# Kernel tuning notes

Hardware: AMD Instinct MI355X
Metric: run time of the kernel (lower is better)

The kernel has to match this reference:

```python
import jax, jax.numpy as jnp
import numpy as np

N = 100000          # nodes
E = 3200000         # edges
C_IN = 64
HIDDEN = 64
NUM_CLASSES = 10
NUM_GRAPHS = 256
EPS = 1e-5


def _graph_conv(x, src, dst, w_rel, w_root, b):
    # PyG GraphConv(aggr='mean'): out_i = W_rel * mean_{j->i} x_j + W_root * x_i + b
    msg_sum = jax.ops.segment_sum(x[src], dst, num_segments=N)            # [N, C]
    cnt = jax.ops.segment_sum(jnp.ones((src.shape[0], 1), x.dtype), dst,
                              num_segments=N)                             # [N, 1]
    agg = msg_sum / jnp.maximum(cnt, 1.0)
    return agg @ w_rel + x @ w_root + b


def _batch_norm(x, gamma, beta):
    # PyG BatchNorm in training mode: batch stats over the node dimension
    mean = jnp.mean(x, axis=0)
    var = jnp.var(x, axis=0)
    return (x - mean) * jax.lax.rsqrt(var + EPS) * gamma + beta


def setup_inputs() -> dict:
    key = jax.random.key(0)
    ks = jax.random.split(key, 20)
    x = jax.random.normal(ks[0], (N, C_IN), dtype=jnp.float32)
    edge_index = jax.random.randint(ks[1], (2, E), 0, N, dtype=jnp.int32)
    batch = jnp.sort(jax.random.randint(ks[2], (N,), 0, NUM_GRAPHS, dtype=jnp.int32))

    def lin(k, fan_in, fan_out):
        s = 1.0 / np.sqrt(fan_in)
        return jax.random.uniform(k, (fan_in, fan_out), jnp.float32, -s, s)

    dims = [(C_IN, 16), (16, 32), (32, 32), (32, HIDDEN)]
    params = {}
    ki = 3
    for i, (ci, co) in enumerate(dims, start=1):
        params[f"w_rel{i}"] = lin(ks[ki], ci, co); ki += 1
        params[f"w_root{i}"] = lin(ks[ki], ci, co); ki += 1
        params[f"b{i}"] = jnp.zeros((co,), jnp.float32)
        params[f"g{i}"] = jnp.ones((co,), jnp.float32)
        params[f"be{i}"] = jnp.zeros((co,), jnp.float32)
    params["w_lin1"] = lin(ks[ki], HIDDEN, HIDDEN); ki += 1
    params["b_lin1"] = jnp.zeros((HIDDEN,), jnp.float32)
    params["w_lin2"] = lin(ks[ki], HIDDEN, NUM_CLASSES); ki += 1
    params["b_lin2"] = jnp.zeros((NUM_CLASSES,), jnp.float32)

    return {"x": x, "edge_index": edge_index, "batch": batch, **params}


def reference(x, edge_index, batch,
              w_rel1, w_root1, b1, g1, be1,
              w_rel2, w_root2, b2, g2, be2,
              w_rel3, w_root3, b3, g3, be3,
              w_rel4, w_root4, b4, g4, be4,
              w_lin1, b_lin1, w_lin2, b_lin2):
    src, dst = edge_index[0], edge_index[1]
    h = jax.nn.elu(_batch_norm(_graph_conv(x, src, dst, w_rel1, w_root1, b1), g1, be1))
    h = jax.nn.elu(_batch_norm(_graph_conv(h, src, dst, w_rel2, w_root2, b2), g2, be2))
    h = jax.nn.elu(_batch_norm(_graph_conv(h, src, dst, w_rel3, w_root3, b3), g3, be3))
    h = jax.nn.elu(_batch_norm(_graph_conv(h, src, dst, w_rel4, w_root4, b4), g4, be4))
    # global mean pool over graphs
    pooled = jax.ops.segment_sum(h, batch, num_segments=NUM_GRAPHS)
    cnt = jax.ops.segment_sum(jnp.ones((N, 1), h.dtype), batch, num_segments=NUM_GRAPHS)
    pooled = pooled / jnp.maximum(cnt, 1.0)
    z = jax.nn.relu(pooled @ w_lin1 + b_lin1)
    # dropout omitted (deterministic / eval mode)
    logits = z @ w_lin2 + b_lin2
    return jax.nn.log_softmax(logits, axis=-1)
```

## Files before the change

kernel.cpp:

```cpp
#include <hip/hip_runtime.h>
#include <hip/hip_bf16.h>
#include <math.h>

#define NGRAPHS 256
#define BSHIFT 8
#define NBUCK 512
#define NSORT 256
#define SBLK 256
#define SMASK 0x00FFFFFFu

__device__ __forceinline__ float bf2f(unsigned short u) {
    return __uint_as_float((unsigned)u << 16);
}
__device__ __forceinline__ unsigned short f2bf(float f) {
    unsigned u = __float_as_uint(f);
    unsigned r = (u + 0x7FFFu + ((u >> 16) & 1u)) >> 16;
    return (unsigned short)r;
}

__global__ __launch_bounds__(256) void k_bhist(const int* __restrict__ dst, int* __restrict__ hmat, int E) {
    __shared__ int hist[NBUCK];
    for (int i = threadIdx.x; i < NBUCK; i += 256) hist[i] = 0;
    __syncthreads();
    int chunk = (E + NSORT - 1) / NSORT;
    int lo = blockIdx.x * chunk;
    int hi = lo + chunk; if (hi > E) hi = E;
    for (int i = lo + threadIdx.x; i < hi; i += 256) {
        int d = __builtin_nontemporal_load(dst + i);
        atomicAdd(&hist[d >> BSHIFT], 1);
    }
    __syncthreads();
    for (int i = threadIdx.x; i < NBUCK; i += 256)
        hmat[(size_t)blockIdx.x * NBUCK + i] = hist[i];
}

__global__ __launch_bounds__(256) void k_cscan(int* __restrict__ hmat, int* __restrict__ btot) {
    int col = blockIdx.x * 256 + threadIdx.x;
    int run = 0;
#pragma unroll 4
    for (int r = 0; r < NSORT; r++) {
        int v = hmat[(size_t)r * NBUCK + col];
        hmat[(size_t)r * NBUCK + col] = run;
        run += v;
    }
    btot[col] = run;
}

__global__ __launch_bounds__(512) void k_bscan(const int* __restrict__ btot, int* __restrict__ bstart) {
    __shared__ int s[512];
    int tid = threadIdx.x;
    int v = btot[tid];
    s[tid] = v;
    __syncthreads();
    for (int off = 1; off < 512; off <<= 1) {
        int t = (tid >= off) ? s[tid - off] : 0;
        __syncthreads();
        s[tid] += t;
        __syncthreads();
    }
    bstart[tid] = s[tid] - v;
    if (tid == 511) bstart[NBUCK] = s[511];
}

__global__ __launch_bounds__(256) void k_bscatter(const int* __restrict__ src, const int* __restrict__ dst,
                                                  const int* __restrict__ hmat, const int* __restrict__ bstart,
                                                  unsigned* __restrict__ ebuf, int E) {
    __shared__ int cur[NBUCK];
    for (int i = threadIdx.x; i < NBUCK; i += 256)
        cur[i] = bstart[i] + hmat[(size_t)blockIdx.x * NBUCK + i];
    __syncthreads();
    int chunk = (E + NSORT - 1) / NSORT;
    int lo = blockIdx.x * chunk;
    int hi = lo + chunk; if (hi > E) hi = E;
    for (int i = lo + threadIdx.x; i < hi; i += 256) {
        int d = __builtin_nontemporal_load(dst + i);
        int s = __builtin_nontemporal_load(src + i);
        int p = atomicAdd(&cur[d >> BSHIFT], 1);
        ebuf[p] = (unsigned)s | ((unsigned)(d & 255) << 24);
    }
}

__global__ __launch_bounds__(256) void k_sort2(const unsigned* __restrict__ ebuf, const int* __restrict__ bstart,
                                               int* __restrict__ csr, int* __restrict__ row_start, int N) {
    __shared__ int hist[256];
    __shared__ int sc[256];
    __shared__ int scur[256];
    int b = blockIdx.x;
    int e0 = bstart[b], e1 = bstart[b + 1];
    hist[threadIdx.x] = 0;
    __syncthreads();
    for (int i = e0 + threadIdx.x; i < e1; i += 256)
        atomicAdd(&hist[__builtin_nontemporal_load(ebuf + i) >> 24], 1);
    __syncthreads();
    sc[threadIdx.x] = hist[threadIdx.x];
    __syncthreads();
    for (int off = 1; off < 256; off <<= 1) {
        int t = (threadIdx.x >= off) ? sc[threadIdx.x - off] : 0;
        __syncthreads();
        sc[threadIdx.x] += t;
        __syncthreads();
    }
    {
        int inc = sc[threadIdx.x];
        int ex = inc - hist[threadIdx.x];
        scur[threadIdx.x] = e0 + ex;
        int node = (b << BSHIFT) + threadIdx.x;
        if (node < N) row_start[node] = e0 + ex;
        if (node == N - 1) row_start[N] = e0 + inc;
    }
    __syncthreads();
    for (int i = e0 + threadIdx.x; i < e1; i += 256) {
        unsigned w = __builtin_nontemporal_load(ebuf + i);
        int p = atomicAdd(&scur[w >> 24], 1);
        csr[p] = (int)(w & SMASK);
    }
}

template <int CI, int CO, bool HAS_REL, bool HAS_ROOT, bool ADD_AGG, bool HAS_BIAS, bool IN_BF16, bool OUT_BF16>
__global__ __launch_bounds__(256) void k_lin(const void* __restrict__ hroot_v, const float* __restrict__ hrel,
                                             const float* __restrict__ w_rel, const float* __restrict__ w_root,
                                             const float* __restrict__ bias, const float* __restrict__ aggadd,
                                             float* __restrict__ out, unsigned short* __restrict__ outb, int N) {
    constexpr int QPR = CO / 4;
    __shared__ float s_rel[HAS_REL ? CI * CO : 1];
    __shared__ float s_root[HAS_ROOT ? CI * CO : 1];
    __shared__ float s_b[HAS_BIAS ? CO : 4];
    if (HAS_REL)
        for (int i = threadIdx.x; i < CI * CO; i += 256) s_rel[i] = w_rel[i];
    if (HAS_ROOT)
        for (int i = threadIdx.x; i < CI * CO; i += 256) s_root[i] = w_root[i];
    if (HAS_BIAS && threadIdx.x < CO) s_b[threadIdx.x] = bias[threadIdx.x];
    __syncthreads();

    int t = blockIdx.x * 256 + threadIdx.x;
    int n = t / QPR;
    int c0 = (t % QPR) * 4;
    if (n >= N) return;

    float rr[HAS_ROOT ? CI : 1];
    if (HAS_ROOT) {
        if (IN_BF16) {
            const ushort4* hp = (const ushort4*)((const unsigned short*)hroot_v + (size_t)n * CI);
#pragma unroll
            for (int i = 0; i < CI / 4; i++) {
                ushort4 v = hp[i];
                rr[4 * i + 0] = bf2f(v.x); rr[4 * i + 1] = bf2f(v.y);
                rr[4 * i + 2] = bf2f(v.z); rr[4 * i + 3] = bf2f(v.w);
            }
        } else {
            const float4* hp = (const float4*)((const float*)hroot_v + (size_t)n * CI);
#pragma unroll
            for (int i = 0; i < CI / 4; i++) {
                float4 v = hp[i];
                rr[4 * i + 0] = v.x; rr[4 * i + 1] = v.y; rr[4 * i + 2] = v.z; rr[4 * i + 3] = v.w;
            }
        }
    }
    float ar[HAS_REL ? CI : 1];
    if (HAS_REL) {
        const float4* mp = (const float4*)(hrel + (size_t)n * CI);
#pragma unroll
        for (int i = 0; i < CI / 4; i++) {
            float4 v = mp[i];
            ar[4 * i + 0] = v.x; ar[4 * i + 1] = v.y; ar[4 * i + 2] = v.z; ar[4 * i + 3] = v.w;
        }
    }

    float4 acc;
    if (HAS_BIAS) acc = *(const float4*)&s_b[c0];
    else { acc.x = 0.f; acc.y = 0.f; acc.z = 0.f; acc.w = 0.f; }
    if (ADD_AGG) {
        float4 v = *(const float4*)(aggadd + (size_t)n * CO + c0);
        acc.x += v.x; acc.y += v.y; acc.z += v.z; acc.w += v.w;
    }

#pragma unroll
    for (int ci = 0; ci < CI; ci++) {
        if (HAS_REL) {
            float a = ar[ci];
            float4 w = *(const float4*)&s_rel[ci * CO + c0];
            acc.x += a * w.x; acc.y += a * w.y; acc.z += a * w.z; acc.w += a * w.w;
        }
        if (HAS_ROOT) {
            float hv = rr[ci];
            float4 w = *(const float4*)&s_root[ci * CO + c0];
            acc.x += hv * w.x; acc.y += hv * w.y; acc.z += hv * w.z; acc.w += hv * w.w;
        }
    }
    if (OUT_BF16) {
        ushort4 o;
        o.x = f2bf(acc.x); o.y = f2bf(acc.y); o.z = f2bf(acc.z); o.w = f2bf(acc.w);
        *(ushort4*)(outb + (size_t)n * CO + c0) = o;
    } else {
        *(float4*)(out + (size_t)n * CO + c0) = acc;
    }
}

#define GCHUNK 1024
template <int C>
__global__ __launch_bounds__(256) void k_gather(const unsigned short* __restrict__ h,
                                                const int* __restrict__ row_start,
                                                const int* __restrict__ csr, float* __restrict__ agg, int N) {
    constexpr int LPR = C / 4;
    constexpr int EPP = 64 / LPR;
    constexpr int DEPTH = 32 / EPP;
    __shared__ int sbuf[GCHUNK];
    int lane = threadIdx.x & 63;
    int w = threadIdx.x >> 6;
    int nb = blockIdx.x * 4;
    int wid = nb + w;
    bool act = wid < N;
    int nb_end = nb + 4; if (nb_end > N) nb_end = N;
    int eb0 = row_start[nb];
    int eb1 = row_start[nb_end];
    int r0 = act ? row_start[wid] : 0;
    int r1 = act ? row_start[wid + 1] : 0;
    int es = lane / LPR;
    int cq = (lane % LPR) * 4;

    float a0 = 0.f, a1 = 0.f, a2 = 0.f, a3 = 0.f;
    for (int base = eb0; base < eb1; base += GCHUNK) {
        int len = eb1 - base; if (len > GCHUNK) len = GCHUNK;
        __syncthreads();
        for (int i = threadIdx.x; i < len; i += 256)
            sbuf[i] = __builtin_nontemporal_load(csr + base + i);
        __syncthreads();
        if (act) {
            int lo = (r0 > base ? r0 : base) - base;
            int hiv = r1 < base + len ? r1 : base + len;
            int hi = hiv - base;
            if (hi > lo) {
                int nfull = (hi - lo) >> 5;
                int j0 = lo;
                for (int b = 0; b < nfull; b++, j0 += 32) {
                    int s[DEPTH];
#pragma unroll
                    for (int u = 0; u < DEPTH; u++) s[u] = sbuf[j0 + u * EPP + es];
                    ushort4 v[DEPTH];
#pragma unroll
                    for (int u = 0; u < DEPTH; u++)
                        v[u] = *(const ushort4*)(h + (size_t)s[u] * C + cq);
#pragma unroll
                    for (int u = 0; u < DEPTH; u++) {
                        a0 += bf2f(v[u].x); a1 += bf2f(v[u].y);
                        a2 += bf2f(v[u].z); a3 += bf2f(v[u].w);
                    }
                }
                for (int j = j0 + es; j < hi; j += EPP) {
                    int s = sbuf[j];
                    ushort4 v = *(const ushort4*)(h + (size_t)s * C + cq);
                    a0 += bf2f(v.x); a1 += bf2f(v.y); a2 += bf2f(v.z); a3 += bf2f(v.w);
                }
            }
        }
    }
#pragma unroll
    for (int off = LPR; off < 64; off <<= 1) {
        a0 += __shfl_xor(a0, off, 64);
        a1 += __shfl_xor(a1, off, 64);
        a2 += __shfl_xor(a2, off, 64);
        a3 += __shfl_xor(a3, off, 64);
    }
    if (act && lane < LPR) {
        int deg = r1 - r0;
        float rec = 1.0f / (float)(deg > 0 ? deg : 1);
        float4 o; o.x = a0 * rec; o.y = a1 * rec; o.z = a2 * rec; o.w = a3 * rec;
        *(float4*)(agg + (size_t)wid * C + cq) = o;
    }
}

template <int CO>
__global__ __launch_bounds__(256) void k_stats(const float* __restrict__ h, float* __restrict__ partials,
                                               const float* __restrict__ g, const float* __restrict__ be,
                                               float* __restrict__ stats, int* __restrict__ cnt,
                                               float invN, int N) {
    constexpr int QPR = CO / 4;
    __shared__ float part[4][2 * CO];
    __shared__ float red[128];
    __shared__ int is_last;
    int total = N * QPR;
    float s0 = 0, s1 = 0, s2 = 0, s3 = 0, q0 = 0, q1 = 0, q2 = 0, q3 = 0;
    int idx = blockIdx.x * 256 + threadIdx.x;
    for (int i = idx; i < total; i += SBLK * 256) {
        float4 v = ((const float4*)h)[i];
        s0 += v.x; q0 += v.x * v.x;
        s1 += v.y; q1 += v.y * v.y;
        s2 += v.z; q2 += v.z * v.z;
        s3 += v.w; q3 += v.w * v.w;
    }
#pragma unroll
    for (int off = QPR; off < 64; off <<= 1) {
        s0 += __shfl_xor(s0, off, 64); q0 += __shfl_xor(q0, off, 64);
        s1 += __shfl_xor(s1, off, 64); q1 += __shfl_xor(q1, off, 64);
        s2 += __shfl_xor(s2, off, 64); q2 += __shfl_xor(q2, off, 64);
        s3 += __shfl_xor(s3, off, 64); q3 += __shfl_xor(q3, off, 64);
    }
    int lane = threadIdx.x & 63;
    int w = threadIdx.x >> 6;
    if (lane < QPR) {
        int cq = lane * 4;
        part[w][cq + 0] = s0; part[w][CO + cq + 0] = q0;
        part[w][cq + 1] = s1; part[w][CO + cq + 1] = q1;
        part[w][cq + 2] = s2; part[w][CO + cq + 2] = q2;
        part[w][cq + 3] = s3; part[w][CO + cq + 3] = q3;
    }
    __syncthreads();
    if (threadIdx.x < 2 * CO) {
        float v = part[0][threadIdx.x] + part[1][threadIdx.x] + part[2][threadIdx.x] + part[3][threadIdx.x];
        partials[blockIdx.x * (2 * CO) + threadIdx.x] = v;
    }
    __threadfence();
    if (threadIdx.x == 0) is_last = (atomicAdd(cnt, 1) == SBLK - 1);
    __syncthreads();
    if (!is_last) return;
    __threadfence();
    int c = threadIdx.x;
    if (c < 2 * CO) {
        float s = 0.f;
        for (int b = 0; b < SBLK; b++) s += partials[b * 2 * CO + c];
        red[c] = s;
    }
    __syncthreads();
    if (c < CO) {
        float mean = red[c] * invN;
        float var = red[CO + c] * invN - mean * mean;
        float sc = g[c] * rsqrtf(var + 1e-5f);
        stats[128 + c] = sc;
        stats[192 + c] = be[c] - mean * sc;
    }
}

template <int CO>
__global__ __launch_bounds__(256) void k_bn_elu(const float* __restrict__ h, const float* __restrict__ stats,
                                                unsigned short* __restrict__ hb, int N) {
    __shared__ float sc[CO], sh[CO];
    if (threadIdx.x < CO) {
        sc[threadIdx.x] = stats[128 + threadIdx.x];
        sh[threadIdx.x] = stats[192 + threadIdx.x];
    }
    __syncthreads();
    int total = N * (CO / 4);
    int i = blockIdx.x * 256 + threadIdx.x;
    if (i >= total) return;
    float4 v = ((const float4*)h)[i];
    int cq = (i % (CO / 4)) * 4;
    v.x = v.x * sc[cq + 0] + sh[cq + 0];
    v.y = v.y * sc[cq + 1] + sh[cq + 1];
    v.z = v.z * sc[cq + 2] + sh[cq + 2];
    v.w = v.w * sc[cq + 3] + sh[cq + 3];
    v.x = v.x > 0.f ? v.x : expm1f(v.x);
    v.y = v.y > 0.f ? v.y : expm1f(v.y);
    v.z = v.z > 0.f ? v.z : expm1f(v.z);
    v.w = v.w > 0.f ? v.w : expm1f(v.w);
    ushort4 o;
    o.x = f2bf(v.x); o.y = f2bf(v.y); o.z = f2bf(v.z); o.w = f2bf(v.w);
    ((ushort4*)hb)[i] = o;
}

__global__ __launch_bounds__(256) void k_bn_elu_pool(const float* __restrict__ h, const float* __restrict__ stats,
                                                     const int* __restrict__ batch,
                                                     float* __restrict__ pooled, float* __restrict__ cntg, int N) {
    int lane = threadIdx.x & 63;
    int wid = blockIdx.x * 4 + (threadIdx.x >> 6);
    int n0 = wid * 16;
    if (n0 >= N) return;
    float scl = stats[128 + lane];
    float shl = stats[192 + lane];
    int nmax = N - n0; if (nmax > 16) nmax = 16;
    int cur = batch[n0];
    float acc = 0.f;
    float run = 0.f;
    for (int k = 0; k < nmax; k++) {
        int g = batch[n0 + k];
        if (g != cur) {
            atomicAdd(&pooled[(size_t)cur * 64 + lane], acc);
            if (lane == 0) atomicAdd(&cntg[cur], run);
            cur = g; acc = 0.f; run = 0.f;
        }
        float v = h[(size_t)(n0 + k) * 64 + lane] * scl + shl;
        v = v > 0.f ? v : expm1f(v);
        acc += v;
        run += 1.f;
    }
    atomicAdd(&pooled[(size_t)cur * 64 + lane], acc);
    if (lane == 0) atomicAdd(&cntg[cur], run);
}

__global__ __launch_bounds__(256) void k_head(const float* __restrict__ pooled, const float* __restrict__ cntg,
                                              const float* __restrict__ w1, const float* __restrict__ b1,
                                              const float* __restrict__ w2, const float* __restrict__ b2,
                                              float* __restrict__ out) {
    int g = threadIdx.x;
    float rec = 1.0f / fmaxf(cntg[g], 1.0f);
    float p[64];
    {
        const float4* pp = (const float4*)(pooled + (size_t)g * 64);
#pragma unroll
        for (int i = 0; i < 16; i++) {
            float4 v = pp[i];
            p[4 * i + 0] = v.x * rec; p[4 * i + 1] = v.y * rec;
            p[4 * i + 2] = v.z * rec; p[4 * i + 3] = v.w * rec;
        }
    }
    float lg[10];
#pragma unroll
    for (int t = 0; t < 10; t++) lg[t] = b2[t];
#pragma unroll 1
    for (int j = 0; j < 64; j++) {
        float a = b1[j];
#pragma unroll
        for (int k = 0; k < 64; k++) a += p[k] * w1[k * 64 + j];
        a = fmaxf(a, 0.f);
#pragma unroll
        for (int t = 0; t < 10; t++) lg[t] += a * w2[j * 10 + t];
    }
    float m = -1e30f;
#pragma unroll
    for (int t = 0; t < 10; t++) m = fmaxf(m, lg[t]);
    float s = 0.f;
#pragma unroll
    for (int t = 0; t < 10; t++) s += expf(lg[t] - m);
    float lse = m + logf(s);
#pragma unroll
    for (int t = 0; t < 10; t++) out[(size_t)g * 10 + t] = lg[t] - lse;
}

extern "C" void kernel_launch(void* const* d_in, const int* in_sizes, int n_in,
                              void* d_out, int out_size, void* d_ws, size_t ws_size,
                              hipStream_t stream) {
    const float* x = (const float*)d_in[0];
    const int* ei = (const int*)d_in[1];
    const int* batch = (const int*)d_in[2];
    const int N = in_sizes[0] / 64;
    const int E = in_sizes[1] / 2;
    const int* src = ei;
    const int* dst = ei + E;

    const float* w_rel1 = (const float*)d_in[3];
    const float* w_root1 = (const float*)d_in[4];
    const float* b1 = (const float*)d_in[5];
    const float* g1 = (const float*)d_in[6];
    const float* be1 = (const float*)d_in[7];
    const float* w_rel2 = (const float*)d_in[8];
    const float* w_root2 = (const float*)d_in[9];
    const float* b2 = (const float*)d_in[10];
    const float* g2 = (const float*)d_in[11];
    const float* be2 = (const float*)d_in[12];
    const float* w_rel3 = (const float*)d_in[13];
    const float* w_root3 = (const float*)d_in[14];
    const float* b3 = (const float*)d_in[15];
    const float* g3 = (const float*)d_in[16];
    const float* be3 = (const float*)d_in[17];
    const float* w_rel4 = (const float*)d_in[18];
    const float* w_root4 = (const float*)d_in[19];
    const float* b4 = (const float*)d_in[20];
    const float* g4 = (const float*)d_in[21];
    const float* be4 = (const float*)d_in[22];
    const float* w_lin1 = (const float*)d_in[23];
    const float* b_lin1 = (const float*)d_in[24];
    const float* w_lin2 = (const float*)d_in[25];
    const float* b_lin2 = (const float*)d_in[26];

    char* ws = (char*)d_ws;
    size_t off = 0;
    auto alloc = [&](size_t bytes) { size_t o = off; off += (bytes + 255) & ~(size_t)255; return o; };
    int* hmat = (int*)(ws + alloc((size_t)NSORT * NBUCK * 4));
    int* btot = (int*)(ws + alloc((size_t)NBUCK * 4));
    int* bstart = (int*)(ws + alloc((size_t)(NBUCK + 1) * 4));
    unsigned* ebuf = (unsigned*)(ws + alloc((size_t)E * 4));
    int* csr = (int*)(ws + alloc((size_t)E * 4));
    int* row_start = (int*)(ws + alloc((size_t)(N + 1) * 4));
    float* agg = (float*)(ws + alloc((size_t)N * 32 * 4));
    unsigned short* y1b = (unsigned short*)(ws + alloc((size_t)N * 16 * 2));
    unsigned short* hb = (unsigned short*)(ws + alloc((size_t)N * 64 * 2));
    float* bufA = (float*)(ws + alloc((size_t)N * 64 * 4));
    float* stats = (float*)(ws + alloc(4 * 256 * 4));
    float* partials = (float*)(ws + alloc((size_t)SBLK * 128 * 4));
    float* pooled = (float*)(ws + alloc((size_t)(NGRAPHS * 64 + NGRAPHS + 8) * 4));
    float* cntg = pooled + NGRAPHS * 64;
    int* cnt = (int*)(cntg + NGRAPHS);

    hipMemsetAsync(pooled, 0, (size_t)(NGRAPHS * 64 + NGRAPHS + 8) * 4, stream);

    const float invN = 1.0f / (float)N;
    const int gbl = (N + 3) / 4;
    auto lgrid = [&](int qpr) { return (N * qpr + 255) / 256; };

    k_bhist<<<NSORT, 256, 0, stream>>>(dst, hmat, E);
    k_cscan<<<NBUCK / 256, 256, 0, stream>>>(hmat, btot);
    k_bscan<<<1, 512, 0, stream>>>(btot, bstart);
    k_bscatter<<<NSORT, 256, 0, stream>>>(src, dst, hmat, bstart, ebuf, E);
    k_sort2<<<NBUCK, 256, 0, stream>>>(ebuf, bstart, csr, row_start, N);

    k_lin<64, 16, true, false, false, false, false, true><<<lgrid(4), 256, 0, stream>>>(
        nullptr, x, w_rel1, nullptr, nullptr, nullptr, nullptr, y1b, N);
    k_gather<16><<<gbl, 256, 0, stream>>>(y1b, row_start, csr, agg, N);
    k_lin<64, 16, false, true, true, true, false, false><<<lgrid(4), 256, 0, stream>>>(
        x, nullptr, nullptr, w_root1, b1, agg, bufA, nullptr, N);
    k_stats<16><<<SBLK, 256, 0, stream>>>(bufA, partials, g1, be1, stats + 0, cnt + 0, invN, N);
    k_bn_elu<16><<<(N * 4 + 255) / 256, 256, 0, stream>>>(bufA, stats + 0, hb, N);

    k_gather<16><<<gbl, 256, 0, stream>>>(hb, row_start, csr, agg, N);
    k_lin<16, 32, true, true, false, true, true, false><<<lgrid(8), 256, 0, stream>>>(
        hb, agg, w_rel2, w_root2, b2, nullptr, bufA, nullptr, N);
    k_stats<32><<<SBLK, 256, 0, stream>>>(bufA, partials, g2, be2, stats + 256, cnt + 1, invN, N);
    k_bn_elu<32><<<(N * 8 + 255) / 256, 256, 0, stream>>>(bufA, stats + 256, hb, N);

    k_gather<32><<<gbl, 256, 0, stream>>>(hb, row_start, csr, agg, N);
    k_lin<32, 32, true, true, false, true, true, false><<<lgrid(8), 256, 0, stream>>>(
        hb, agg, w_rel3, w_root3, b3, nullptr, bufA, nullptr, N);
    k_stats<32><<<SBLK, 256, 0, stream>>>(bufA, partials, g3, be3, stats + 512, cnt + 2, invN, N);
    k_bn_elu<32><<<(N * 8 + 255) / 256, 256, 0, stream>>>(bufA, stats + 512, hb, N);

    k_gather<32><<<gbl, 256, 0, stream>>>(hb, row_start, csr, agg, N);
    k_lin<32, 64, true, true, false, true, true, false><<<lgrid(16), 256, 0, stream>>>(
        hb, agg, w_rel4, w_root4, b4, nullptr, bufA, nullptr, N);
    k_stats<64><<<SBLK, 256, 0, stream>>>(bufA, partials, g4, be4, stats + 768, cnt + 3, invN, N);
    int waves16 = (N + 15) / 16;
    k_bn_elu_pool<<<(waves16 + 3) / 4, 256, 0, stream>>>(bufA, stats + 768, batch, pooled, cntg, N);

    k_head<<<1, 256, 0, stream>>>(pooled, cntg, w_lin1, b_lin1, w_lin2, b_lin2, (float*)d_out);
}
```

Before: 638.9 us.

## Fuse BN stats into linear kernels, merge scans, head into pool, drop memset

Computes BatchNorm sum and sum-of-squares inside the linear kernel, which now runs as a grid-stride loop over 512 blocks, so the separate stats pass that re-read the layer output is gone. The column and bucket scans become one kernel, the memset is moved into the histogram kernel's first block, and the head MLP runs in the last block of the pooling kernel. The gather loop is also rewritten with predicated batches of four. This cuts launches and one full read of each layer output, at the cost of a persistent-grid linear kernel with less parallelism and a serial last-block reduction.

```diff
diff --git a/kernel.cpp b/kernel.cpp
--- a/kernel.cpp
+++ b/kernel.cpp
@@ -6,7 +6,7 @@
 #define BSHIFT 8
 #define NBUCK 512
 #define NSORT 256
-#define SBLK 256
+#define LSTAT 512
 #define SMASK 0x00FFFFFFu
 
 __device__ __forceinline__ float bf2f(unsigned short u) {
@@ -18,7 +18,11 @@
     return (unsigned short)r;
 }
 
-__global__ __launch_bounds__(256) void k_bhist(const int* __restrict__ dst, int* __restrict__ hmat, int E) {
+__global__ __launch_bounds__(256) void k_bhist(const int* __restrict__ dst, int* __restrict__ hmat, int E,
+                                               float* __restrict__ zbase, int zwords) {
+    if (blockIdx.x == 0) {
+        for (int i = threadIdx.x; i < zwords; i += 256) zbase[i] = 0.f;
+    }
     __shared__ int hist[NBUCK];
     for (int i = threadIdx.x; i < NBUCK; i += 256) hist[i] = 0;
     __syncthreads();
@@ -34,8 +38,9 @@
         hmat[(size_t)blockIdx.x * NBUCK + i] = hist[i];
 }
 
-__global__ __launch_bounds__(256) void k_cscan(int* __restrict__ hmat, int* __restrict__ btot) {
-    int col = blockIdx.x * 256 + threadIdx.x;
+__global__ __launch_bounds__(512) void k_scan(int* __restrict__ hmat, int* __restrict__ bstart) {
+    __shared__ int s[512];
+    int col = threadIdx.x;
     int run = 0;
 #pragma unroll 4
     for (int r = 0; r < NSORT; r++) {
@@ -43,23 +48,16 @@
         hmat[(size_t)r * NBUCK + col] = run;
         run += v;
     }
-    btot[col] = run;
-}
-
-__global__ __launch_bounds__(512) void k_bscan(const int* __restrict__ btot, int* __restrict__ bstart) {
-    __shared__ int s[512];
-    int tid = threadIdx.x;
-    int v = btot[tid];
-    s[tid] = v;
+    s[col] = run;
     __syncthreads();
     for (int off = 1; off < 512; off <<= 1) {
-        int t = (tid >= off) ? s[tid - off] : 0;
+        int t = (col >= off) ? s[col - off] : 0;
         __syncthreads();
-        s[tid] += t;
+        s[col] += t;
         __syncthreads();
     }
-    bstart[tid] = s[tid] - v;
-    if (tid == 511) bstart[NBUCK] = s[511];
+    bstart[col] = s[col] - run;
+    if (col == 511) bstart[NBUCK] = s[511];
 }
 
 __global__ __launch_bounds__(256) void k_bscatter(const int* __restrict__ src, const int* __restrict__ dst,
@@ -116,83 +114,151 @@
     }
 }
 
-template <int CI, int CO, bool HAS_REL, bool HAS_ROOT, bool ADD_AGG, bool HAS_BIAS, bool IN_BF16, bool OUT_BF16>
-__global__ __launch_bounds__(256) void k_lin(const void* __restrict__ hroot_v, const float* __restrict__ hrel,
-                                             const float* __restrict__ w_rel, const float* __restrict__ w_root,
-                                             const float* __restrict__ bias, const float* __restrict__ aggadd,
-                                             float* __restrict__ out, unsigned short* __restrict__ outb, int N) {
+template <int CI, int CO>
+__global__ __launch_bounds__(256) void k_lin_rel(const float* __restrict__ hrel, const float* __restrict__ w_rel,
+                                                 unsigned short* __restrict__ outb, int N) {
     constexpr int QPR = CO / 4;
-    __shared__ float s_rel[HAS_REL ? CI * CO : 1];
-    __shared__ float s_root[HAS_ROOT ? CI * CO : 1];
-    __shared__ float s_b[HAS_BIAS ? CO : 4];
-    if (HAS_REL)
-        for (int i = threadIdx.x; i < CI * CO; i += 256) s_rel[i] = w_rel[i];
-    if (HAS_ROOT)
-        for (int i = threadIdx.x; i < CI * CO; i += 256) s_root[i] = w_root[i];
-    if (HAS_BIAS && threadIdx.x < CO) s_b[threadIdx.x] = bias[threadIdx.x];
-    __syncthreads();
-
+    __shared__ float s_rel[CI * CO];
+    for (int i = threadIdx.x; i < CI * CO; i += 256) s_rel[i] = w_rel[i];
+    __syncthreads();
     int t = blockIdx.x * 256 + threadIdx.x;
     int n = t / QPR;
     int c0 = (t % QPR) * 4;
     if (n >= N) return;
-
-    float rr[HAS_ROOT ? CI : 1];
-    if (HAS_ROOT) {
+    float ar[CI];
+    const float4* mp = (const float4*)(hrel + (size_t)n * CI);
+#pragma unroll
+    for (int i = 0; i < CI / 4; i++) {
+        float4 v = mp[i];
+        ar[4 * i + 0] = v.x; ar[4 * i + 1] = v.y; ar[4 * i + 2] = v.z; ar[4 * i + 3] = v.w;
+    }
+    float4 acc; acc.x = 0.f; acc.y = 0.f; acc.z = 0.f; acc.w = 0.f;
+#pragma unroll
+    for (int ci = 0; ci < CI; ci++) {
+        float a = ar[ci];
+        float4 w = *(const float4*)&s_rel[ci * CO + c0];
+        acc.x += a * w.x; acc.y += a * w.y; acc.z += a * w.z; acc.w += a * w.w;
+    }
+    ushort4 o;
+    o.x = f2bf(acc.x); o.y = f2bf(acc.y); o.z = f2bf(acc.z); o.w = f2bf(acc.w);
+    *(ushort4*)(outb + (size_t)n * CO + c0) = o;
+}
+
+template <int CI, int CO, bool HAS_REL, bool ADD_AGG, bool IN_BF16>
+__global__ __launch_bounds__(256) void k_lin_stats(const void* __restrict__ hroot_v, const float* __restrict__ hrel,
+                                                   const float* __restrict__ w_rel, const float* __restrict__ w_root,
+                                                   const float* __restrict__ bias, const float* __restrict__ aggadd,
+                                                   float* __restrict__ out, float* __restrict__ partials,
+                                                   const float* __restrict__ g, const float* __restrict__ be,
+                                                   float* __restrict__ stats, int* __restrict__ cnt,
+                                                   float invN, int N) {
+    constexpr int QPR = CO / 4;
+    __shared__ float s_rel[HAS_REL ? CI * CO : 1];
+    __shared__ float s_root[CI * CO];
+    __shared__ float s_b[CO];
+    __shared__ float part[4][2 * CO];
+    __shared__ float red[128];
+    __shared__ int is_last;
+    if (HAS_REL)
+        for (int i = threadIdx.x; i < CI * CO; i += 256) s_rel[i] = w_rel[i];
+    for (int i = threadIdx.x; i < CI * CO; i += 256) s_root[i] = w_root[i];
+    if (threadIdx.x < CO) s_b[threadIdx.x] = bias[threadIdx.x];
+    __syncthreads();
+
+    int total = N * QPR;
+    float s0 = 0, s1 = 0, s2 = 0, s3 = 0, q0 = 0, q1 = 0, q2 = 0, q3 = 0;
+    for (int i = blockIdx.x * 256 + threadIdx.x; i < total; i += LSTAT * 256) {
+        int n = i / QPR;
+        int c0 = (i % QPR) * 4;
+
+        float rr[CI];
         if (IN_BF16) {
             const ushort4* hp = (const ushort4*)((const unsigned short*)hroot_v + (size_t)n * CI);
 #pragma unroll
-            for (int i = 0; i < CI / 4; i++) {
-                ushort4 v = hp[i];
-                rr[4 * i + 0] = bf2f(v.x); rr[4 * i + 1] = bf2f(v.y);
-                rr[4 * i + 2] = bf2f(v.z); rr[4 * i + 3] = bf2f(v.w);
+            for (int k = 0; k < CI / 4; k++) {
+                ushort4 v = hp[k];
+                rr[4 * k + 0] = bf2f(v.x); rr[4 * k + 1] = bf2f(v.y);
+                rr[4 * k + 2] = bf2f(v.z); rr[4 * k + 3] = bf2f(v.w);
             }
         } else {
             const float4* hp = (const float4*)((const float*)hroot_v + (size_t)n * CI);
 #pragma unroll
-            for (int i = 0; i < CI / 4; i++) {
-                float4 v = hp[i];
-                rr[4 * i + 0] = v.x; rr[4 * i + 1] = v.y; rr[4 * i + 2] = v.z; rr[4 * i + 3] = v.w;
+            for (int k = 0; k < CI / 4; k++) {
+                float4 v = hp[k];
+                rr[4 * k + 0] = v.x; rr[4 * k + 1] = v.y; rr[4 * k + 2] = v.z; rr[4 * k + 3] = v.w;
             }
         }
-    }
-    float ar[HAS_REL ? CI : 1];
-    if (HAS_REL) {
-        const float4* mp = (const float4*)(hrel + (size_t)n * CI);
-#pragma unroll
-        for (int i = 0; i < CI / 4; i++) {
-            float4 v = mp[i];
-            ar[4 * i + 0] = v.x; ar[4 * i + 1] = v.y; ar[4 * i + 2] = v.z; ar[4 * i + 3] = v.w;
-        }
-    }
-
-    float4 acc;
-    if (HAS_BIAS) acc = *(const float4*)&s_b[c0];
-    else { acc.x = 0.f; acc.y = 0.f; acc.z = 0.f; acc.w = 0.f; }
-    if (ADD_AGG) {
-        float4 v = *(const float4*)(aggadd + (size_t)n * CO + c0);
-        acc.x += v.x; acc.y += v.y; acc.z += v.z; acc.w += v.w;
-    }
-
-#pragma unroll
-    for (int ci = 0; ci < CI; ci++) {
+        float ar[HAS_REL ? CI : 1];
         if (HAS_REL) {
-            float a = ar[ci];
-            float4 w = *(const float4*)&s_rel[ci * CO + c0];
-            acc.x += a * w.x; acc.y += a * w.y; acc.z += a * w.z; acc.w += a * w.w;
-        }
-        if (HAS_ROOT) {
+            const float4* mp = (const float4*)(hrel + (size_t)n * CI);
+#pragma unroll
+            for (int k = 0; k < CI / 4; k++) {
+                float4 v = mp[k];
+                ar[4 * k + 0] = v.x; ar[4 * k + 1] = v.y; ar[4 * k + 2] = v.z; ar[4 * k + 3] = v.w;
+            }
+        }
+        float4 acc = *(const float4*)&s_b[c0];
+        if (ADD_AGG) {
+            float4 v = ((const float4*)aggadd)[i];
+            acc.x += v.x; acc.y += v.y; acc.z += v.z; acc.w += v.w;
+        }
+#pragma unroll
+        for (int ci = 0; ci < CI; ci++) {
             float hv = rr[ci];
             float4 w = *(const float4*)&s_root[ci * CO + c0];
             acc.x += hv * w.x; acc.y += hv * w.y; acc.z += hv * w.z; acc.w += hv * w.w;
-        }
-    }
-    if (OUT_BF16) {
-        ushort4 o;
-        o.x = f2bf(acc.x); o.y = f2bf(acc.y); o.z = f2bf(acc.z); o.w = f2bf(acc.w);
-        *(ushort4*)(outb + (size_t)n * CO + c0) = o;
-    } else {
-        *(float4*)(out + (size_t)n * CO + c0) = acc;
+            if (HAS_REL) {
+                float a = ar[ci];
+                float4 wr = *(const float4*)&s_rel[ci * CO + c0];
+                acc.x += a * wr.x; acc.y += a * wr.y; acc.z += a * wr.z; acc.w += a * wr.w;
+            }
+        }
+        ((float4*)out)[i] = acc;
+        s0 += acc.x; q0 += acc.x * acc.x;
+        s1 += acc.y; q1 += acc.y * acc.y;
+        s2 += acc.z; q2 += acc.z * acc.z;
+        s3 += acc.w; q3 += acc.w * acc.w;
+    }
+#pragma unroll
+    for (int off = QPR; off < 64; off <<= 1) {
+        s0 += __shfl_xor(s0, off, 64); q0 += __shfl_xor(q0, off, 64);
+        s1 += __shfl_xor(s1, off, 64); q1 += __shfl_xor(q1, off, 64);
+        s2 += __shfl_xor(s2, off, 64); q2 += __shfl_xor(q2, off, 64);
+        s3 += __shfl_xor(s3, off, 64); q3 += __shfl_xor(q3, off, 64);
+    }
+    int lane = threadIdx.x & 63;
+    int w = threadIdx.x >> 6;
+    if (lane < QPR) {
+        int cq = lane * 4;
+        part[w][cq + 0] = s0; part[w][CO + cq + 0] = q0;
+        part[w][cq + 1] = s1; part[w][CO + cq + 1] = q1;
+        part[w][cq + 2] = s2; part[w][CO + cq + 2] = q2;
+        part[w][cq + 3] = s3; part[w][CO + cq + 3] = q3;
+    }
+    __syncthreads();
+    if (threadIdx.x < 2 * CO) {
+        float v = part[0][threadIdx.x] + part[1][threadIdx.x] + part[2][threadIdx.x] + part[3][threadIdx.x];
+        partials[blockIdx.x * (2 * CO) + threadIdx.x] = v;
+    }
+    __threadfence();
+    if (threadIdx.x == 0) is_last = (atomicAdd(cnt, 1) == LSTAT - 1);
+    __syncthreads();
+    if (!is_last) return;
+    __threadfence();
+    int c = threadIdx.x;
+    if (c < 2 * CO) {
+        float s = 0.f;
+#pragma unroll 8
+        for (int b = 0; b < LSTAT; b++) s += partials[b * 2 * CO + c];
+        red[c] = s;
+    }
+    __syncthreads();
+    if (c < CO) {
+        float mean = red[c] * invN;
+        float var = red[CO + c] * invN - mean * mean;
+        float sc = g[c] * rsqrtf(var + 1e-5f);
+        stats[128 + c] = sc;
+        stats[192 + c] = be[c] - mean * sc;
     }
 }
 
@@ -203,7 +269,7 @@
                                                 const int* __restrict__ csr, float* __restrict__ agg, int N) {
     constexpr int LPR = C / 4;
     constexpr int EPP = 64 / LPR;
-    constexpr int DEPTH = 32 / EPP;
+    constexpr int BATCH = 4 * EPP;
     __shared__ int sbuf[GCHUNK];
     int lane = threadIdx.x & 63;
     int w = threadIdx.x >> 6;
@@ -229,27 +295,25 @@
             int lo = (r0 > base ? r0 : base) - base;
             int hiv = r1 < base + len ? r1 : base + len;
             int hi = hiv - base;
-            if (hi > lo) {
-                int nfull = (hi - lo) >> 5;
-                int j0 = lo;
-                for (int b = 0; b < nfull; b++, j0 += 32) {
-                    int s[DEPTH];
-#pragma unroll
-                    for (int u = 0; u < DEPTH; u++) s[u] = sbuf[j0 + u * EPP + es];
-                    ushort4 v[DEPTH];
-#pragma unroll
-                    for (int u = 0; u < DEPTH; u++)
-                        v[u] = *(const ushort4*)(h + (size_t)s[u] * C + cq);
-#pragma unroll
-                    for (int u = 0; u < DEPTH; u++) {
+#pragma unroll 2
+            for (int j0 = lo; j0 < hi; j0 += BATCH) {
+                int s[4]; bool p[4];
+#pragma unroll
+                for (int u = 0; u < 4; u++) {
+                    int j = j0 + u * EPP + es;
+                    p[u] = j < hi;
+                    s[u] = sbuf[p[u] ? j : j0];
+                }
+                ushort4 v[4];
+#pragma unroll
+                for (int u = 0; u < 4; u++)
+                    v[u] = *(const ushort4*)(h + (size_t)s[u] * C + cq);
+#pragma unroll
+                for (int u = 0; u < 4; u++) {
+                    if (p[u]) {
                         a0 += bf2f(v[u].x); a1 += bf2f(v[u].y);
                         a2 += bf2f(v[u].z); a3 += bf2f(v[u].w);
                     }
-                }
-                for (int j = j0 + es; j < hi; j += EPP) {
-                    int s = sbuf[j];
-                    ushort4 v = *(const ushort4*)(h + (size_t)s * C + cq);
-                    a0 += bf2f(v.x); a1 += bf2f(v.y); a2 += bf2f(v.z); a3 += bf2f(v.w);
                 }
             }
         }
@@ -266,67 +330,6 @@
         float rec = 1.0f / (float)(deg > 0 ? deg : 1);
         float4 o; o.x = a0 * rec; o.y = a1 * rec; o.z = a2 * rec; o.w = a3 * rec;
         *(float4*)(agg + (size_t)wid * C + cq) = o;
-    }
-}
-
-template <int CO>
-__global__ __launch_bounds__(256) void k_stats(const float* __restrict__ h, float* __restrict__ partials,
-                                               const float* __restrict__ g, const float* __restrict__ be,
-                                               float* __restrict__ stats, int* __restrict__ cnt,
-                                               float invN, int N) {
-    constexpr int QPR = CO / 4;
-    __shared__ float part[4][2 * CO];
-    __shared__ float red[128];
-    __shared__ int is_last;
-    int total = N * QPR;
-    float s0 = 0, s1 = 0, s2 = 0, s3 = 0, q0 = 0, q1 = 0, q2 = 0, q3 = 0;
-    int idx = blockIdx.x * 256 + threadIdx.x;
-    for (int i = idx; i < total; i += SBLK * 256) {
-        float4 v = ((const float4*)h)[i];
-        s0 += v.x; q0 += v.x * v.x;
-        s1 += v.y; q1 += v.y * v.y;
-        s2 += v.z; q2 += v.z * v.z;
-        s3 += v.w; q3 += v.w * v.w;
-    }
-#pragma unroll
-    for (int off = QPR; off < 64; off <<= 1) {
-        s0 += __shfl_xor(s0, off, 64); q0 += __shfl_xor(q0, off, 64);
-        s1 += __shfl_xor(s1, off, 64); q1 += __shfl_xor(q1, off, 64);
-        s2 += __shfl_xor(s2, off, 64); q2 += __shfl_xor(q2, off, 64);
-        s3 += __shfl_xor(s3, off, 64); q3 += __shfl_xor(q3, off, 64);
-    }
-    int lane = threadIdx.x & 63;
-    int w = threadIdx.x >> 6;
-    if (lane < QPR) {
-        int cq = lane * 4;
-        part[w][cq + 0] = s0; part[w][CO + cq + 0] = q0;
-        part[w][cq + 1] = s1; part[w][CO + cq + 1] = q1;
-        part[w][cq + 2] = s2; part[w][CO + cq + 2] = q2;
-        part[w][cq + 3] = s3; part[w][CO + cq + 3] = q3;
-    }
-    __syncthreads();
-    if (threadIdx.x < 2 * CO) {
-        float v = part[0][threadIdx.x] + part[1][threadIdx.x] + part[2][threadIdx.x] + part[3][threadIdx.x];
-        partials[blockIdx.x * (2 * CO) + threadIdx.x] = v;
-    }
-    __threadfence();
-    if (threadIdx.x == 0) is_last = (atomicAdd(cnt, 1) == SBLK - 1);
-    __syncthreads();
-    if (!is_last) return;
-    __threadfence();
-    int c = threadIdx.x;
-    if (c < 2 * CO) {
-        float s = 0.f;
-        for (int b = 0; b < SBLK; b++) s += partials[b * 2 * CO + c];
-        red[c] = s;
-    }
-    __syncthreads();
-    if (c < CO) {
-        float mean = red[c] * invN;
-        float var = red[CO + c] * invN - mean * mean;
-        float sc = g[c] * rsqrtf(var + 1e-5f);
-        stats[128 + c] = sc;
-        stats[192 + c] = be[c] - mean * sc;
     }
 }
 
@@ -357,39 +360,45 @@
     ((ushort4*)hb)[i] = o;
 }
 
-__global__ __launch_bounds__(256) void k_bn_elu_pool(const float* __restrict__ h, const float* __restrict__ stats,
-                                                     const int* __restrict__ batch,
-                                                     float* __restrict__ pooled, float* __restrict__ cntg, int N) {
+__global__ __launch_bounds__(256) void k_bn_elu_pool_head(const float* __restrict__ h, const float* __restrict__ stats,
+                                                          const int* __restrict__ batch,
+                                                          float* __restrict__ pooled, float* __restrict__ cntg,
+                                                          int* __restrict__ cnt,
+                                                          const float* __restrict__ w1, const float* __restrict__ b1,
+                                                          const float* __restrict__ w2, const float* __restrict__ b2,
+                                                          float* __restrict__ out, int N) {
+    __shared__ int is_last;
     int lane = threadIdx.x & 63;
     int wid = blockIdx.x * 4 + (threadIdx.x >> 6);
     int n0 = wid * 16;
-    if (n0 >= N) return;
-    float scl = stats[128 + lane];
-    float shl = stats[192 + lane];
-    int nmax = N - n0; if (nmax > 16) nmax = 16;
-    int cur = batch[n0];
-    float acc = 0.f;
-    float run = 0.f;
-    for (int k = 0; k < nmax; k++) {
-        int g = batch[n0 + k];
-        if (g != cur) {
-            atomicAdd(&pooled[(size_t)cur * 64 + lane], acc);
-            if (lane == 0) atomicAdd(&cntg[cur], run);
-            cur = g; acc = 0.f; run = 0.f;
-        }
-        float v = h[(size_t)(n0 + k) * 64 + lane] * scl + shl;
-        v = v > 0.f ? v : expm1f(v);
-        acc += v;
-        run += 1.f;
-    }
-    atomicAdd(&pooled[(size_t)cur * 64 + lane], acc);
-    if (lane == 0) atomicAdd(&cntg[cur], run);
-}
-
-__global__ __launch_bounds__(256) void k_head(const float* __restrict__ pooled, const float* __restrict__ cntg,
-                                              const float* __restrict__ w1, const float* __restrict__ b1,
-                                              const float* __restrict__ w2, const float* __restrict__ b2,
-                                              float* __restrict__ out) {
+    if (n0 < N) {
+        float scl = stats[128 + lane];
+        float shl = stats[192 + lane];
+        int nmax = N - n0; if (nmax > 16) nmax = 16;
+        int cur = batch[n0];
+        float acc = 0.f;
+        float run = 0.f;
+        for (int k = 0; k < nmax; k++) {
+            int g = batch[n0 + k];
+            if (g != cur) {
+                atomicAdd(&pooled[(size_t)cur * 64 + lane], acc);
+                if (lane == 0) atomicAdd(&cntg[cur], run);
+                cur = g; acc = 0.f; run = 0.f;
+            }
+            float v = h[(size_t)(n0 + k) * 64 + lane] * scl + shl;
+            v = v > 0.f ? v : expm1f(v);
+            acc += v;
+            run += 1.f;
+        }
+        atomicAdd(&pooled[(size_t)cur * 64 + lane], acc);
+        if (lane == 0) atomicAdd(&cntg[cur], run);
+    }
+    __threadfence();
+    __syncthreads();
+    if (threadIdx.x == 0) is_last = (atomicAdd(cnt, 1) == (int)gridDim.x - 1);
+    __syncthreads();
+    if (!is_last) return;
+    __threadfence();
     int g = threadIdx.x;
     float rec = 1.0f / fmaxf(cntg[g], 1.0f);
     float p[64];
@@ -465,7 +474,6 @@
     size_t off = 0;
     auto alloc = [&](size_t bytes) { size_t o = off; off += (bytes + 255) & ~(size_t)255; return o; };
     int* hmat = (int*)(ws + alloc((size_t)NSORT * NBUCK * 4));
-    int* btot = (int*)(ws + alloc((size_t)NBUCK * 4));
     int* bstart = (int*)(ws + alloc((size_t)(NBUCK + 1) * 4));
     unsigned* ebuf = (unsigned*)(ws + alloc((size_t)E * 4));
     int* csr = (int*)(ws + alloc((size_t)E * 4));
@@ -475,49 +483,40 @@
     unsigned short* hb = (unsigned short*)(ws + alloc((size_t)N * 64 * 2));
     float* bufA = (float*)(ws + alloc((size_t)N * 64 * 4));
     float* stats = (float*)(ws + alloc(4 * 256 * 4));
-    float* partials = (float*)(ws + alloc((size_t)SBLK * 128 * 4));
+    float* partials = (float*)(ws + alloc((size_t)LSTAT * 128 * 4));
     float* pooled = (float*)(ws + alloc((size_t)(NGRAPHS * 64 + NGRAPHS + 8) * 4));
     float* cntg = pooled + NGRAPHS * 64;
     int* cnt = (int*)(cntg + NGRAPHS);
-
-    hipMemsetAsync(pooled, 0, (size_t)(NGRAPHS * 64 + NGRAPHS + 8) * 4, stream);
+    const int zwords = NGRAPHS * 64 + NGRAPHS + 8;
 
     const float invN = 1.0f / (float)N;
     const int gbl = (N + 3) / 4;
-    auto lgrid = [&](int qpr) { return (N * qpr + 255) / 256; };
-
-    k_bhist<<<NSORT, 256, 0, stream>>>(dst, hmat, E);
-    k_cscan<<<NBUCK / 256, 256, 0, stream>>>(hmat, btot);
-    k_bscan<<<1, 512, 0, stream>>>(btot, bstart);
+
+    k_bhist<<<NSORT, 256, 0, stream>>>(dst, hmat, E, pooled, zwords);
+    k_scan<<<1, 512, 0, stream>>>(hmat, bstart);
     k_bscatter<<<NSORT, 256, 0, stream>>>(src, dst, hmat, bstart, ebuf, E);
     k_sort2<<<NBUCK, 256, 0, stream>>>(ebuf, bstart, csr, row_start, N);
 
-    k_lin<64, 16, true, false, false, false, false, true><<<lgrid(4), 256, 0, stream>>>(
-        nullptr, x, w_rel1, nullptr, nullptr, nullptr, nullptr, y1b, N);
+    k_lin_rel<64, 16><<<(N * 4 + 255) / 256, 256, 0, stream>>>(x, w_rel1, y1b, N);
     k_gather<16><<<gbl, 256, 0, stream>>>(y1b, row_start, csr, agg, N);
-    k_lin<64, 16, false, true, true, true, false, false><<<lgrid(4), 256, 0, stream>>>(
-        x, nullptr, nullptr, w_root1, b1, agg, bufA, nullptr, N);
-    k_stats<16><<<SBLK, 256, 0, stream>>>(bufA, partials, g1, be1, stats + 0, cnt + 0, invN, N);
+    k_lin_stats<64, 16, false, true, false><<<LSTAT, 256, 0, stream>>>(
+        x, nullptr, nullptr, w_root1, b1, agg, bufA, partials, g1, be1, stats + 0, cnt + 0, invN, N);
     k_bn_elu<16><<<(N * 4 + 255) / 256, 256, 0, stream>>>(bufA, stats + 0, hb, N);
 
     k_gather<16><<<gbl, 256, 0, stream>>>(hb, row_start, csr, agg, N);
-    k_lin<16, 32, true, true, false, true, true, false><<<lgrid(8), 256, 0, stream>>>(
-        hb, agg, w_rel2, w_root2, b2, nullptr, bufA, nullptr, N);
-    k_stats<32><<<SBLK, 256, 0, stream>>>(bufA, partials, g2, be2, stats + 256, cnt + 1, invN, N);
+    k_lin_stats<16, 32, true, false, true><<<LSTAT, 256, 0, stream>>>(
+        hb, agg, w_rel2, w_root2, b2, nullptr, bufA, partials, g2, be2, stats + 256, cnt + 1, invN, N);
     k_bn_elu<32><<<(N * 8 + 255) / 256, 256, 0, stream>>>(bufA, stats + 256, hb, N);
 
     k_gather<32><<<gbl, 256, 0, stream>>>(hb, row_start, csr, agg, N);
-    k_lin<32, 32, true, true, false, true, true, false><<<lgrid(8), 256, 0, stream>>>(
-        hb, agg, w_rel3, w_root3, b3, nullptr, bufA, nullptr, N);
-    k_stats<32><<<SBLK, 256, 0, stream>>>(bufA, partials, g3, be3, stats + 512, cnt + 2, invN, N);
+    k_lin_stats<32, 32, true, false, true><<<LSTAT, 256, 0, stream>>>(
+        hb, agg, w_rel3, w_root3, b3, nullptr, bufA, partials, g3, be3, stats + 512, cnt + 2, invN, N);
     k_bn_elu<32><<<(N * 8 + 255) / 256, 256, 0, stream>>>(bufA, stats + 512, hb, N);
 
     k_gather<32><<<gbl, 256, 0, stream>>>(hb, row_start, csr, agg, N);
-    k_lin<32, 64, true, true, false, true, true, false><<<lgrid(16), 256, 0, stream>>>(
-        hb, agg, w_rel4, w_root4, b4, nullptr, bufA, nullptr, N);
-    k_stats<64><<<SBLK, 256, 0, stream>>>(bufA, partials, g4, be4, stats + 768, cnt + 3, invN, N);
+    k_lin_stats<32, 64, true, false, true><<<LSTAT, 256, 0, stream>>>(
+        hb, agg, w_rel4, w_root4, b4, nullptr, bufA, partials, g4, be4, stats + 768, cnt + 3, invN, N);
     int waves16 = (N + 15) / 16;
-    k_bn_elu_pool<<<(waves16 + 3) / 4, 256, 0, stream>>>(bufA, stats + 768, batch, pooled, cntg, N);
-
-    k_head<<<1, 256, 0, stream>>>(pooled, cntg, w_lin1, b_lin1, w_lin2, b_lin2, (float*)d_out);
-}
+    k_bn_elu_pool_head<<<(waves16 + 3) / 4, 256, 0, stream>>>(
+        bufA, stats + 768, batch, pooled, cntg, cnt + 4, w_lin1, b_lin1, w_lin2, b_lin2, (float*)d_out, N);
+}
```

Result: slower. 858.5 us (+34.4%).
